# Kernel optimization log

Hardware: AMD Instinct MI355X
Metric: run time of the kernel (lower is better)

Reference implementation:

```python
import jax, jax.numpy as jnp
import numpy as np

N = 100000   # nodes
E = 600000   # edges
SIZES = [128, 128, 128, 64]


def setup_inputs() -> dict:
    key = jax.random.key(0)
    ks = jax.random.split(key, 16)
    x = jax.random.normal(ks[0], (N, SIZES[0]), dtype=jnp.float32)
    edge_index = jax.random.randint(ks[1], (2, E), 0, N, dtype=jnp.int64)
    inp = {"x": x, "edge_index": edge_index}
    ki = 2
    for i in range(3):
        fin, fout = SIZES[i], SIZES[i + 1]
        s = 1.0 / np.sqrt(fin)
        inp[f"Wl{i}"] = jax.random.uniform(ks[ki], (fout, fin), jnp.float32, -s, s); ki += 1
        inp[f"bl{i}"] = jax.random.uniform(ks[ki], (fout,), jnp.float32, -s, s); ki += 1
        inp[f"Wr{i}"] = jax.random.uniform(ks[ki], (fout, fin), jnp.float32, -s, s); ki += 1
    return inp


def _sage(h, src, dst, Wl, bl, Wr):
    # PyG SAGEConv (aggr='mean'): out = lin_l(mean_{j in N(i)} x_j) + lin_r(x_i)
    msg_sum = jax.ops.segment_sum(h[src], dst, num_segments=N)          # [N, fin]
    cnt = jax.ops.segment_sum(jnp.ones((src.shape[0],), h.dtype), dst, num_segments=N)
    mean = msg_sum / jnp.maximum(cnt, 1.0)[:, None]                      # nodes w/o nbrs -> 0
    return mean @ Wl.T + bl + h @ Wr.T


def reference(x, edge_index, Wl0, bl0, Wr0, Wl1, bl1, Wr1, Wl2, bl2, Wr2):
    src, dst = edge_index[0], edge_index[1]
    h = _sage(x, src, dst, Wl0, bl0, Wr0)
    h = jax.nn.relu(h)                 # dropout p=0.0 -> identity
    h = _sage(h, src, dst, Wl1, bl1, Wr1)
    h = jax.nn.relu(h)
    h = _sage(h, src, dst, Wl2, bl2, Wr2)
    return h                            # last_layer='linear' appends nothing
```

## Files before the change

kernel.cpp:

```cpp
#include <hip/hip_runtime.h>

#define NN 100000
#define NE 600000
constexpr int FIN = 128;
constexpr int SCAN_BLOCKS = (NN + 255) / 256;

typedef __attribute__((ext_vector_type(8))) short bf16x8;
typedef __attribute__((ext_vector_type(4))) float f32x4;

__device__ __forceinline__ unsigned packbf2(float a, float b) {
  unsigned ua = __float_as_uint(a); ua += 0x7FFFu + ((ua >> 16) & 1u);
  unsigned ub = __float_as_uint(b); ub += 0x7FFFu + ((ub >> 16) & 1u);
  return (ua >> 16) | (ub & 0xFFFF0000u);
}
__device__ __forceinline__ float lo16f(unsigned u) { return __uint_as_float(u << 16); }
__device__ __forceinline__ float hi16f(unsigned u) { return __uint_as_float(u & 0xFFFF0000u); }

__device__ __forceinline__ void acc8(float* a, const uint4& v) {
  a[0] += lo16f(v.x); a[1] += hi16f(v.x);
  a[2] += lo16f(v.y); a[3] += hi16f(v.y);
  a[4] += lo16f(v.z); a[5] += hi16f(v.z);
  a[6] += lo16f(v.w); a[7] += hi16f(v.w);
}

template <int NCT>
__device__ __forceinline__ void castw_one(int pidx, const float* __restrict__ Wl,
                                          const float* __restrict__ Wr,
                                          short* __restrict__ wpk) {
  int t = pidx & 7;
  int lane = (pidx >> 3) & 63;
  int ks = (pidx >> 9) & 1;
  int c = (pidx >> 10) & (NCT - 1);
  int chunk = pidx >> ((NCT == 8) ? 13 : 12);
  int l15 = lane & 15, lq = lane >> 4;
  int j = c * 16 + l15;
  int k = chunk * 64 + ks * 32 + lq * 8 + t;
  float v = (k < 128) ? Wl[j * 128 + k] : Wr[j * 128 + (k - 128)];
  unsigned u = __float_as_uint(v);
  u += 0x7FFFu + ((u >> 16) & 1u);
  wpk[pidx] = (short)(u >> 16);
}

__global__ __launch_bounds__(256) void k_prep(
    const float* __restrict__ Wl0, const float* __restrict__ Wr0,
    const float* __restrict__ Wl1, const float* __restrict__ Wr1,
    const float* __restrict__ Wl2, const float* __restrict__ Wr2,
    short* __restrict__ wpk_all, float4* __restrict__ dc,
    const float* __restrict__ x, short* __restrict__ xb) {
  const int b = blockIdx.x;
  if (b < 320) {
    int pidx = b * 256 + threadIdx.x;
    if (pidx < 32768) castw_one<8>(pidx, Wl0, Wr0, wpk_all);
    else if (pidx < 65536) castw_one<8>(pidx - 32768, Wl1, Wr1, wpk_all + 32768);
    else castw_one<4>(pidx - 65536, Wl2, Wr2, wpk_all + 65536);
  } else if (b < 516) {
    int i = (b - 320) * 256 + threadIdx.x;
    if (i < 2 * NN / 4) dc[i] = make_float4(0.f, 0.f, 0.f, 0.f);
  } else {
    int i = (b - 516) * 256 + threadIdx.x;
    if (i < NN * FIN / 8) {
      const float4 v0 = *reinterpret_cast<const float4*>(x + (size_t)i * 8);
      const float4 v1 = *reinterpret_cast<const float4*>(x + (size_t)i * 8 + 4);
      uint4 o;
      o.x = packbf2(v0.x, v0.y);
      o.y = packbf2(v0.z, v0.w);
      o.z = packbf2(v1.x, v1.y);
      o.w = packbf2(v1.z, v1.w);
      *reinterpret_cast<uint4*>(xb + (size_t)i * 8) = o;
    }
  }
}


__global__ __launch_bounds__(256) void k_count(const int* __restrict__ dst,
                                               int* __restrict__ deg) {
  int e = blockIdx.x * blockDim.x + threadIdx.x;
  if (e < NE) {
    int d = dst[e];
    if ((unsigned)d < NN) atomicAdd(&deg[d], 1);
  }
}

__global__ __launch_bounds__(256) void k_scan1(const int* __restrict__ deg,
                                               int* __restrict__ rowptr,
                                               int* __restrict__ bsum,
                                               float* __restrict__ inv) {
  __shared__ int s[256];
  int i = blockIdx.x * 256 + threadIdx.x;
  int v = (i < NN) ? deg[i] : 0;
  s[threadIdx.x] = v;
  if (i < NN) inv[i] = 1.0f / fmaxf((float)v, 1.0f);
  __syncthreads();
#pragma unroll
  for (int off = 1; off < 256; off <<= 1) {
    int t = (threadIdx.x >= off) ? s[threadIdx.x - off] : 0;
    __syncthreads();
    s[threadIdx.x] += t;
    __syncthreads();
  }
  if (i < NN) rowptr[i + 1] = s[threadIdx.x];
  if (threadIdx.x == 255) bsum[blockIdx.x] = s[255];
}

__global__ __launch_bounds__(512) void k_scan2(int* __restrict__ bsum, int nb) {
  __shared__ int s[512];
  int v = (threadIdx.x < nb) ? bsum[threadIdx.x] : 0;
  s[threadIdx.x] = v;
  __syncthreads();
#pragma unroll
  for (int off = 1; off < 512; off <<= 1) {
    int t = (threadIdx.x >= off) ? s[threadIdx.x - off] : 0;
    __syncthreads();
    s[threadIdx.x] += t;
    __syncthreads();
  }
  if (threadIdx.x < nb) bsum[threadIdx.x] = s[threadIdx.x];
}

__global__ __launch_bounds__(256) void k_scan3(const int* __restrict__ bsum,
                                               int* __restrict__ rowptr) {
  int i = blockIdx.x * 256 + threadIdx.x;
  if (i < NN && blockIdx.x > 0) rowptr[i + 1] += bsum[blockIdx.x - 1];
  if (i == 0) rowptr[0] = 0;
}

__global__ __launch_bounds__(256) void k_fill(const int* __restrict__ src,
                                              const int* __restrict__ dst,
                                              const int* __restrict__ rowptr,
                                              int* __restrict__ cursor,
                                              int* __restrict__ adj) {
  int e = blockIdx.x * blockDim.x + threadIdx.x;
  if (e < NE) {
    int d = dst[e];
    int s = src[e];
    if ((unsigned)d < NN && (unsigned)s < NN) {
      int pos = atomicAdd(&cursor[d], 1);
      adj[rowptr[d] + pos] = s;
    }
  }
}

__global__ __launch_bounds__(256, 8) void k_gather2(
    const int* __restrict__ rowptr, const int* __restrict__ adj,
    const short* __restrict__ hb, const float* __restrict__ inv,
    short* __restrict__ mb) {
  const int node = blockIdx.x * 16 + (threadIdx.x >> 4);
  const int l15 = threadIdx.x & 15;
  if (node >= NN) return;
  const int beg = rowptr[node];
  const int end = rowptr[node + 1];
  const float s = inv[node];
  float a[8] = {0.f, 0.f, 0.f, 0.f, 0.f, 0.f, 0.f, 0.f};
  int e = beg;
  for (; e + 3 < end; e += 4) {
    int s0 = adj[e], s1 = adj[e + 1], s2 = adj[e + 2], s3 = adj[e + 3];
    uint4 v0 = *reinterpret_cast<const uint4*>(hb + (size_t)s0 * FIN + l15 * 8);
    uint4 v1 = *reinterpret_cast<const uint4*>(hb + (size_t)s1 * FIN + l15 * 8);
    uint4 v2 = *reinterpret_cast<const uint4*>(hb + (size_t)s2 * FIN + l15 * 8);
    uint4 v3 = *reinterpret_cast<const uint4*>(hb + (size_t)s3 * FIN + l15 * 8);
    acc8(a, v0); acc8(a, v1); acc8(a, v2); acc8(a, v3);
  }
  for (; e < end; ++e) {
    uint4 v = *reinterpret_cast<const uint4*>(hb + (size_t)adj[e] * FIN + l15 * 8);
    acc8(a, v);
  }
  uint4 o;
  o.x = packbf2(a[0] * s, a[1] * s);
  o.y = packbf2(a[2] * s, a[3] * s);
  o.z = packbf2(a[4] * s, a[5] * s);
  o.w = packbf2(a[6] * s, a[7] * s);
  *reinterpret_cast<uint4*>(mb + (size_t)node * FIN + l15 * 8) = o;
}

template <int FOUT, bool RELU, bool WF32, bool WB16>
__global__ __launch_bounds__(512, 2) void k_gemm2(
    const short* __restrict__ hb, const short* __restrict__ mb,
    const short* __restrict__ wpk, const float* __restrict__ bias,
    float* __restrict__ out, short* __restrict__ outb) {
  constexpr int NCT = FOUT / 16;
  constexpr int NFR = NCT * 4 * 2;
  __shared__ short wlds[NFR * 64 * 8];
  const int lane = threadIdx.x & 63;
  const int w = threadIdx.x >> 6;
  const int l15 = lane & 15;
  const int lq = lane >> 4;
  const int n0 = (blockIdx.x * 8 + w) * 16;
  const int row = n0 + l15;
  const bool ok = row < NN;

#pragma unroll
  for (int i = 0; i < NFR / 8; ++i) {
    int idx = i * 512 + threadIdx.x;
    reinterpret_cast<uint4*>(wlds)[idx] =
        reinterpret_cast<const uint4*>(wpk)[idx];
  }

  bf16x8 am[4], as_[4];
  {
    const short* mp = mb + (size_t)row * FIN + lq * 8;
    const short* sp = hb + (size_t)row * FIN + lq * 8;
#pragma unroll
    for (int q = 0; q < 4; ++q) {
      const int o = (q >> 1) * 64 + (q & 1) * 32;
      if (ok) {
        am[q] = *reinterpret_cast<const bf16x8*>(mp + o);
        as_[q] = *reinterpret_cast<const bf16x8*>(sp + o);
      } else {
#pragma unroll
        for (int i = 0; i < 8; ++i) { am[q][i] = 0; as_[q][i] = 0; }
      }
    }
  }

  __syncthreads();

  f32x4 acc[NCT];
#pragma unroll
  for (int c = 0; c < NCT; ++c)
#pragma unroll
    for (int q = 0; q < 4; ++q) acc[c][q] = 0.f;

#pragma unroll
  for (int chunk = 0; chunk < 4; ++chunk) {
    const bf16x8 a0 = (chunk < 2) ? am[chunk * 2 + 0] : as_[(chunk - 2) * 2 + 0];
    const bf16x8 a1 = (chunk < 2) ? am[chunk * 2 + 1] : as_[(chunk - 2) * 2 + 1];
#pragma unroll
    for (int c = 0; c < NCT; ++c) {
      const bf16x8 b0 = *reinterpret_cast<const bf16x8*>(
          &wlds[(((chunk * NCT + c) * 2 + 0) * 64 + lane) * 8]);
      const bf16x8 b1 = *reinterpret_cast<const bf16x8*>(
          &wlds[(((chunk * NCT + c) * 2 + 1) * 64 + lane) * 8]);
      acc[c] = __builtin_amdgcn_mfma_f32_16x16x32_bf16(b0, a0, acc[c], 0, 0, 0);
      acc[c] = __builtin_amdgcn_mfma_f32_16x16x32_bf16(b1, a1, acc[c], 0, 0, 0);
    }
  }

#pragma unroll
  for (int c = 0; c < NCT; ++c) {
    const f32x4 bb = *reinterpret_cast<const f32x4*>(bias + c * 16 + lq * 4);
    if (ok) {
      f32x4 v = acc[c] + bb;
      if (RELU) {
#pragma unroll
        for (int q = 0; q < 4; ++q) v[q] = fmaxf(v[q], 0.f);
      }
      if (WF32)
        *reinterpret_cast<f32x4*>(out + (size_t)row * FOUT + c * 16 + lq * 4) = v;
      if (WB16) {
        uint2 o;
        o.x = packbf2(v[0], v[1]);
        o.y = packbf2(v[2], v[3]);
        *reinterpret_cast<uint2*>(outb + (size_t)row * FOUT + c * 16 + lq * 4) = o;
      }
    }
  }
}


static inline size_t align512(size_t x) { return (x + 511) & ~(size_t)511; }

extern "C" void kernel_launch(void* const* d_in, const int* in_sizes, int n_in,
                              void* d_out, int out_size, void* d_ws, size_t ws_size,
                              hipStream_t stream) {
  const float* x   = (const float*)d_in[0];
  const int*   ei  = (const int*)d_in[1];
  const float* Wl0 = (const float*)d_in[2];
  const float* bl0 = (const float*)d_in[3];
  const float* Wr0 = (const float*)d_in[4];
  const float* Wl1 = (const float*)d_in[5];
  const float* bl1 = (const float*)d_in[6];
  const float* Wr1 = (const float*)d_in[7];
  const float* Wl2 = (const float*)d_in[8];
  const float* bl2 = (const float*)d_in[9];
  const float* Wr2 = (const float*)d_in[10];
  float* out = (float*)d_out;

  char* ws = (char*)d_ws;
  size_t off = 0;
  float* inv     = (float*)(ws + off); off = align512(off + (size_t)NN * 4);
  short* xb      = (short*)(ws + off); off = align512(off + (size_t)NN * FIN * 2);
  short* hb1     = (short*)(ws + off); off = align512(off + (size_t)NN * FIN * 2);
  short* hb2     = (short*)(ws + off); off = align512(off + (size_t)NN * FIN * 2);
  short* mb      = (short*)(ws + off); off = align512(off + (size_t)NN * FIN * 2);
  short* wpk_all = (short*)(ws + off); off = align512(off + (size_t)(32768 + 32768 + 16384) * 2);
  int*   deg     = (int*)(ws + off);
  int*   cursor  = deg + NN;           off = align512(off + (size_t)2 * NN * 4);
  int*   rowptr  = (int*)(ws + off);   off = align512(off + (size_t)(NN + 1) * 4);
  int*   bsum    = (int*)(ws + off);   off = align512(off + (size_t)SCAN_BLOCKS * 4);
  int*   adj     = (int*)(ws + off);   off = align512(off + (size_t)NE * 4);

  short* wpk0 = wpk_all;
  short* wpk1 = wpk_all + 32768;
  short* wpk2 = wpk_all + 65536;

  const int* srcp = ei;
  const int* dstp = ei + NE;

  const int gather_blocks = (NN + 15) / 16;
  const int gemm_blocks = (NN + 127) / 128;
  const int prep_blocks = 320 + 196 + 6250;

  k_prep<<<prep_blocks, 256, 0, stream>>>(Wl0, Wr0, Wl1, Wr1, Wl2, Wr2,
                                          wpk_all, (float4*)deg, x, xb);

  k_count<<<(NE + 255) / 256, 256, 0, stream>>>(dstp, deg);
  k_scan1<<<SCAN_BLOCKS, 256, 0, stream>>>(deg, rowptr, bsum, inv);
  k_scan2<<<1, 512, 0, stream>>>(bsum, SCAN_BLOCKS);
  k_scan3<<<SCAN_BLOCKS, 256, 0, stream>>>(bsum, rowptr);
  k_fill<<<(NE + 255) / 256, 256, 0, stream>>>(srcp, dstp, rowptr, cursor, adj);

  k_gather2<<<gather_blocks, 256, 0, stream>>>(rowptr, adj, xb, inv, mb);
  k_gemm2<128, true, false, true><<<gemm_blocks, 512, 0, stream>>>(
      xb, mb, wpk0, bl0, nullptr, hb1);

  k_gather2<<<gather_blocks, 256, 0, stream>>>(rowptr, adj, hb1, inv, mb);
  k_gemm2<128, true, false, true><<<gemm_blocks, 512, 0, stream>>>(
      hb1, mb, wpk1, bl1, nullptr, hb2);

  k_gather2<<<gather_blocks, 256, 0, stream>>>(rowptr, adj, hb2, inv, mb);
  k_gemm2<64, false, true, false><<<gemm_blocks, 512, 0, stream>>>(
      hb2, mb, wpk2, bl2, out, nullptr);
}
```

Measured before the change: 223.8 us.

## Balance gather work by edges using binary search over rowptr

Replaces the node-per-16-lane gather launch with an edge-balanced partition. Each block owns a fixed range of 96 edges and finds the nodes whose rows start in that range with two binary searches over rowptr. Its 16 lane groups then loop over those nodes. This targets load imbalance from uneven node degrees, at the cost of two serial binary searches per block (about 17 dependent loads each) and a loop that may leave some lane groups idle.

New measurement: 251.6 us. 12.4% more time.

```diff
diff --git a/kernel.cpp b/kernel.cpp
--- a/kernel.cpp
+++ b/kernel.cpp
@@ -4,6 +4,8 @@
 #define NE 600000
 constexpr int FIN = 128;
 constexpr int SCAN_BLOCKS = (NN + 255) / 256;
+constexpr int EPB = 96;
+constexpr int GATHER_BLOCKS = (NE + EPB - 1) / EPB;
 
 typedef __attribute__((ext_vector_type(8))) short bf16x8;
 typedef __attribute__((ext_vector_type(4))) float f32x4;
@@ -140,36 +142,57 @@
   }
 }
 
-__global__ __launch_bounds__(256, 8) void k_gather2(
+__device__ __forceinline__ int lb_rowptr(const int* __restrict__ rp, int val) {
+  int lo = 0, hi = NN;
+  while (lo < hi) {
+    int mid = (lo + hi) >> 1;
+    if (rp[mid] < val) lo = mid + 1; else hi = mid;
+  }
+  return lo;
+}
+
+__global__ __launch_bounds__(256, 8) void k_gather3(
     const int* __restrict__ rowptr, const int* __restrict__ adj,
     const short* __restrict__ hb, const float* __restrict__ inv,
     short* __restrict__ mb) {
-  const int node = blockIdx.x * 16 + (threadIdx.x >> 4);
+  const int b = blockIdx.x;
+  const int lo = b * EPB;
+  const int hi = (b == GATHER_BLOCKS - 1) ? (NE + 1) : (lo + EPB);
+  const int first = lb_rowptr(rowptr, lo);
+  int last = lb_rowptr(rowptr, hi);
+  if (last > NN) last = NN;
+  const int cnt = last - first;
+  if (cnt <= 0) return;
+
+  const int qid = threadIdx.x >> 4;
   const int l15 = threadIdx.x & 15;
-  if (node >= NN) return;
-  const int beg = rowptr[node];
-  const int end = rowptr[node + 1];
-  const float s = inv[node];
-  float a[8] = {0.f, 0.f, 0.f, 0.f, 0.f, 0.f, 0.f, 0.f};
-  int e = beg;
-  for (; e + 3 < end; e += 4) {
-    int s0 = adj[e], s1 = adj[e + 1], s2 = adj[e + 2], s3 = adj[e + 3];
-    uint4 v0 = *reinterpret_cast<const uint4*>(hb + (size_t)s0 * FIN + l15 * 8);
-    uint4 v1 = *reinterpret_cast<const uint4*>(hb + (size_t)s1 * FIN + l15 * 8);
-    uint4 v2 = *reinterpret_cast<const uint4*>(hb + (size_t)s2 * FIN + l15 * 8);
-    uint4 v3 = *reinterpret_cast<const uint4*>(hb + (size_t)s3 * FIN + l15 * 8);
-    acc8(a, v0); acc8(a, v1); acc8(a, v2); acc8(a, v3);
-  }
-  for (; e < end; ++e) {
-    uint4 v = *reinterpret_cast<const uint4*>(hb + (size_t)adj[e] * FIN + l15 * 8);
-    acc8(a, v);
-  }
-  uint4 o;
-  o.x = packbf2(a[0] * s, a[1] * s);
-  o.y = packbf2(a[2] * s, a[3] * s);
-  o.z = packbf2(a[4] * s, a[5] * s);
-  o.w = packbf2(a[6] * s, a[7] * s);
-  *reinterpret_cast<uint4*>(mb + (size_t)node * FIN + l15 * 8) = o;
+
+  for (int it = qid; it < cnt; it += 16) {
+    const int node = first + it;
+    const int beg = rowptr[node];
+    const int end = rowptr[node + 1];
+    const float s = inv[node];
+    float a[8] = {0.f, 0.f, 0.f, 0.f, 0.f, 0.f, 0.f, 0.f};
+    int e = beg;
+    for (; e + 3 < end; e += 4) {
+      int s0 = adj[e], s1 = adj[e + 1], s2 = adj[e + 2], s3 = adj[e + 3];
+      uint4 v0 = *reinterpret_cast<const uint4*>(hb + (size_t)s0 * FIN + l15 * 8);
+      uint4 v1 = *reinterpret_cast<const uint4*>(hb + (size_t)s1 * FIN + l15 * 8);
+      uint4 v2 = *reinterpret_cast<const uint4*>(hb + (size_t)s2 * FIN + l15 * 8);
+      uint4 v3 = *reinterpret_cast<const uint4*>(hb + (size_t)s3 * FIN + l15 * 8);
+      acc8(a, v0); acc8(a, v1); acc8(a, v2); acc8(a, v3);
+    }
+    for (; e < end; ++e) {
+      uint4 v = *reinterpret_cast<const uint4*>(hb + (size_t)adj[e] * FIN + l15 * 8);
+      acc8(a, v);
+    }
+    uint4 o;
+    o.x = packbf2(a[0] * s, a[1] * s);
+    o.y = packbf2(a[2] * s, a[3] * s);
+    o.z = packbf2(a[4] * s, a[5] * s);
+    o.w = packbf2(a[6] * s, a[7] * s);
+    *reinterpret_cast<uint4*>(mb + (size_t)node * FIN + l15 * 8) = o;
+  }
 }
 
 template <int FOUT, bool RELU, bool WF32, bool WB16>
@@ -296,7 +319,6 @@
   const int* srcp = ei;
   const int* dstp = ei + NE;
 
-  const int gather_blocks = (NN + 15) / 16;
   const int gemm_blocks = (NN + 127) / 128;
   const int prep_blocks = 320 + 196 + 6250;
 
@@ -309,15 +331,15 @@
   k_scan3<<<SCAN_BLOCKS, 256, 0, stream>>>(bsum, rowptr);
   k_fill<<<(NE + 255) / 256, 256, 0, stream>>>(srcp, dstp, rowptr, cursor, adj);
 
-  k_gather2<<<gather_blocks, 256, 0, stream>>>(rowptr, adj, xb, inv, mb);
+  k_gather3<<<GATHER_BLOCKS, 256, 0, stream>>>(rowptr, adj, xb, inv, mb);
   k_gemm2<128, true, false, true><<<gemm_blocks, 512, 0, stream>>>(
       xb, mb, wpk0, bl0, nullptr, hb1);
 
-  k_gather2<<<gather_blocks, 256, 0, stream>>>(rowptr, adj, hb1, inv, mb);
+  k_gather3<<<GATHER_BLOCKS, 256, 0, stream>>>(rowptr, adj, hb1, inv, mb);
   k_gemm2<128, true, false, true><<<gemm_blocks, 512, 0, stream>>>(
       hb1, mb, wpk1, bl1, nullptr, hb2);
 
-  k_gather2<<<gather_blocks, 256, 0, stream>>>(rowptr, adj, hb2, inv, mb);
+  k_gather3<<<GATHER_BLOCKS, 256, 0, stream>>>(rowptr, adj, hb2, inv, mb);
   k_gemm2<64, false, true, false><<<gemm_blocks, 512, 0, stream>>>(
       hb2, mb, wpk2, bl2, out, nullptr);
 }
```
